# Optimization experiments

Measured on AMD Instinct MI355X. Metric: run time of the kernel, lower is better.

## Reference

```python
import jax, jax.numpy as jnp
import numpy as np

N, E = 10000, 160000          # nodes, edges
MUL = 128                     # channel multiplicity of 0e and 1o blocks
NSP = 10                      # node_attrs (species one-hot) dim
NRAD = 8                      # edge_feats radial basis dim
SILU_C = 1.6790               # e3nn normalize2mom constant for SiLU
AVG_NEIGH = 16.0
SQ3 = np.sqrt(3.0).astype(np.float32)


def setup_inputs() -> dict:
    key = jax.random.key(0)
    ks = jax.random.split(key, 14)
    d = {}
    d["node_feats"] = jax.random.normal(ks[0], (N, 4 * MUL), jnp.float32)   # [N, 128 + 128*3]
    d["node_attrs"] = jax.random.normal(ks[1], (N, NSP), jnp.float32)
    d["edge_feats"] = jax.random.normal(ks[2], (E, NRAD), jnp.float32)
    d["edge_attrs"] = jax.random.normal(ks[3], (E, 4), jnp.float32)          # [0e | 1o]
    d["edge_index"] = jax.random.randint(ks[4], (2, E), 0, N, jnp.int32)
    # e3nn internal weights are standard normal; normalization applied in forward
    d["lin1_ws"] = jax.random.normal(ks[5], (MUL, MUL), jnp.float32)
    d["lin1_wv"] = jax.random.normal(ks[6], (MUL, MUL), jnp.float32)
    d["fc_w0"] = jax.random.normal(ks[7], (NRAD, 64), jnp.float32)
    d["fc_w1"] = jax.random.normal(ks[8], (64, 64), jnp.float32)
    d["fc_w2"] = jax.random.normal(ks[9], (64, 4 * MUL), jnp.float32)        # tp.weight_numel = 512
    d["lin2_ws"] = jax.random.normal(ks[10], (2 * MUL, MUL), jnp.float32)    # 256x0e -> 128x0e
    d["lin2_wv"] = jax.random.normal(ks[11], (2 * MUL, MUL), jnp.float32)    # 256x1o -> 128x1o
    d["sc_ws"] = jax.random.normal(ks[12], (MUL, NSP, MUL), jnp.float32)
    d["sc_wv"] = jax.random.normal(ks[13], (MUL, NSP, MUL), jnp.float32)
    return d


def _fc(ef, w0, w1, w2):
    # e3nn FullyConnectedNet: x @ W / sqrt(fan_in), normalize2mom-scaled SiLU between layers
    h = SILU_C * jax.nn.silu(ef @ w0 / np.float32(np.sqrt(NRAD)))
    h = SILU_C * jax.nn.silu(h @ w1 / np.float32(8.0))
    return h @ w2 / np.float32(8.0)


def reference(node_feats, node_attrs, edge_feats, edge_attrs, edge_index,
              lin1_ws, lin1_wv, fc_w0, fc_w1, fc_w2,
              lin2_ws, lin2_wv, sc_ws, sc_wv):
    x_s = node_feats[:, :MUL]                       # [N, 128] scalar block
    x_v = node_feats[:, MUL:].reshape(N, MUL, 3)    # [N, 128, 3] vector block

    # self-connection: FullyConnectedTensorProduct with 10x0e attrs; path weight 1/sqrt(mul1*mul2)
    sc_norm = np.float32(1.0 / np.sqrt(MUL * NSP))
    sc_s = jnp.einsum('nu,nv,uvw->nw', x_s, node_attrs, sc_ws) * sc_norm
    sc_v = jnp.einsum('nuc,nv,uvw->nwc', x_v, node_attrs, sc_wv) * sc_norm

    # linear_1 (per-irrep channel mixing, fan_in = 128)
    l1 = np.float32(1.0 / np.sqrt(MUL))
    y_s = (x_s @ lin1_ws) * l1
    y_v = jnp.einsum('nuc,uw->nwc', x_v, lin1_wv) * l1

    src = edge_index[1]
    dst = edge_index[0]
    xs_e = y_s[src]                                 # [E, 128]
    xv_e = y_v[src]                                 # [E, 128, 3]
    a_s = edge_attrs[:, :1]                         # [E, 1]
    a_v = edge_attrs[:, 1:]                         # [E, 3]

    w = _fc(edge_feats, fc_w0, fc_w1, fc_w2)        # [E, 512]
    w_ss, w_sv, w_vs, w_vv = jnp.split(w, 4, axis=1)  # instruction order in source

    # 'uvu' weighted tensor product with e3nn component/element normalization:
    # net coefficient per path works out to 1 except 1o x 1o -> 0e which is 1/sqrt(3)
    mid_s0 = w_ss * xs_e * a_s                                          # 0e*0e->0e
    mid_s1 = w_vv * jnp.einsum('euc,ec->eu', xv_e, a_v) / SQ3           # 1o*1o->0e
    mid_v2 = (w_sv * xs_e)[:, :, None] * a_v[:, None, :]                # 0e*1o->1o
    mid_v3 = w_vs[:, :, None] * xv_e * a_s[:, :, None]                  # 1o*0e->1o

    inv = np.float32(1.0 / np.sqrt(AVG_NEIGH))
    s = jax.ops.segment_sum(jnp.concatenate([mid_s0, mid_s1], axis=1), dst, num_segments=N) * inv  # [N, 256]
    v = jax.ops.segment_sum(jnp.concatenate([mid_v2, mid_v3], axis=1), dst, num_segments=N) * inv  # [N, 256, 3]

    # linear_2 (fan_in = 256)
    l2 = np.float32(1.0 / np.sqrt(2 * MUL))
    out_s = (s @ lin2_ws) * l2 + sc_s
    out_v = jnp.einsum('nuc,uw->nwc', v, lin2_wv) * l2 + sc_v

    return jnp.concatenate([out_s, out_v.reshape(N, 3 * MUL)], axis=1)   # [N, 512]
```

## Files before the change

kernel.cpp:

```cpp
#include <hip/hip_runtime.h>
#include <hip/hip_bf16.h>
#include <math.h>

#define N_NODES 10000
#define N_EDGES 160000
#define SO_BLK 157
#define VO_BLK 469

typedef __attribute__((ext_vector_type(8))) short short8x;
typedef __attribute__((ext_vector_type(4))) float floatx4;
typedef __attribute__((ext_vector_type(4))) unsigned int uint4x;
typedef __attribute__((ext_vector_type(2))) unsigned int uint2x;

union S8 { short8x v; unsigned short u[8]; uint4 q; uint4x qx; };
union U2 { uint2x v; unsigned short us[4]; };

__device__ __forceinline__ unsigned short f2bf(float x) {
    unsigned int u = __float_as_uint(x);
    return (unsigned short)((u + 0x7fffu + ((u >> 16) & 1u)) >> 16);
}
__device__ __forceinline__ float bf2f(unsigned short u) {
    return __uint_as_float(((unsigned)u) << 16);
}
__device__ __forceinline__ float silu_c(float x) {
    return 1.679f * x / (1.0f + __expf(-x));
}

__global__ __launch_bounds__(256) void pack_all_kernel(
    const float* __restrict__ sc_ws, const float* __restrict__ lin2_ws,
    const float* __restrict__ sc_wv, const float* __restrict__ lin2_wv,
    const float* __restrict__ fc_w2, const float* __restrict__ fc_w1,
    const float* __restrict__ lin1_ws, const float* __restrict__ lin1_wv,
    unsigned short* __restrict__ b_pre, unsigned short* __restrict__ w2a,
    unsigned short* __restrict__ w1a, unsigned short* __restrict__ b_lin)
{
    const int bid = blockIdx.x;
    const int t = threadIdx.x;
    if (bid < 192) {
        int id = bid * 256 + t;
        int mat = id / 24576;
        int slot = id - mat * 24576;
        int ks = slot >> 9;
        int rr = slot & 511;
        int lane = rr & 63;
        int quad = lane >> 4;
        int n = ((rr >> 6) << 4) + (lane & 15);
        const float* sc  = mat ? sc_wv  : sc_ws;
        const float* lin = mat ? lin2_wv : lin2_ws;
        S8 pk;
        #pragma unroll
        for (int j = 0; j < 8; j++) {
            int k = ks * 32 + quad * 8 + j;
            float w;
            if (k < 1280) {
                int u = k & 127, v = k >> 7;
                w = sc[(u * 10 + v) * 128 + n];
            } else {
                w = lin[(k - 1280) * 128 + n];
            }
            pk.u[j] = f2bf(w);
        }
        *(uint4*)(b_pre + (size_t)id * 8) = pk.q;
    } else if (bid < 208) {
        int id = (bid - 192) * 256 + t;
        int lane = id & 63;
        int mfg = (id >> 6) & 31;
        int ks = id >> 11;
        int col = mfg * 16 + (lane & 15);
        int k0 = ks * 32 + (lane >> 4) * 8;
        S8 pk;
        #pragma unroll
        for (int j = 0; j < 8; j++)
            pk.u[j] = f2bf(fc_w2[(k0 + j) * 512 + col] * 0.125f);
        *(uint4*)(w2a + (size_t)id * 8) = pk.q;
    } else if (bid < 210) {
        int id = (bid - 208) * 256 + t;
        int lane = id & 63;
        int mf = (id >> 6) & 3;
        int ks = id >> 8;
        int m = mf * 16 + (lane & 15);
        int k0 = ks * 32 + (lane >> 4) * 8;
        S8 pk;
        #pragma unroll
        for (int j = 0; j < 8; j++)
            pk.u[j] = f2bf(fc_w1[(k0 + j) * 64 + m] * 0.125f);
        *(uint4*)(w1a + (size_t)id * 8) = pk.q;
    } else {
        int id = (bid - 210) * 256 + t;
        int mat = id >> 11;
        int slot = id & 2047;
        int ks = slot >> 9;
        int rr = slot & 511;
        int nf = rr >> 6;
        int lane = rr & 63;
        int n = nf * 16 + (lane & 15);
        int k0 = ks * 32 + (lane >> 4) * 8;
        const float* w = mat ? lin1_wv : lin1_ws;
        const float l1 = 0.0883883476483f;
        S8 pk;
        #pragma unroll
        for (int j = 0; j < 8; j++)
            pk.u[j] = f2bf(w[(k0 + j) * 128 + n] * l1);
        *(uint4*)(b_lin + (size_t)id * 8) = pk.q;
    }
}

__global__ __launch_bounds__(256) void node_lin1_mfma(
    const float* __restrict__ node_feats,
    const unsigned short* __restrict__ b_lin,
    unsigned short* __restrict__ y_pk,
    unsigned short* __restrict__ xvP16)
{
    __shared__ __align__(16) unsigned char smem[32768];
    short8x* Al = (short8x*)smem;
    unsigned short* Yt = (unsigned short*)smem;

    const int blk = blockIdx.x;
    const int t = threadIdx.x;
    const int base = blk * 32;
    const int lane = t & 63;
    const int wv = t >> 6;
    const int m15 = lane & 15;
    const int k0q = (lane >> 4) * 8;

    #pragma unroll
    for (int it = 0; it < 8; it++) {
        int g = wv * 8 + it;
        int af = g >> 2;
        int ks = g & 3;
        int m = af * 16 + m15;
        int comp = m >> 5;
        int nloc = m & 31;
        int node = base + nloc;
        int valid = (node < N_NODES);
        if (!valid) node = N_NODES - 1;
        int k0 = ks * 32 + k0q;
        const float* row = node_feats + (size_t)node * 512;
        S8 pk;
        if (comp == 0) {
            float4 a = *(const float4*)&row[k0];
            float4 b = *(const float4*)&row[k0 + 4];
            pk.u[0] = f2bf(a.x); pk.u[1] = f2bf(a.y); pk.u[2] = f2bf(a.z); pk.u[3] = f2bf(a.w);
            pk.u[4] = f2bf(b.x); pk.u[5] = f2bf(b.y); pk.u[6] = f2bf(b.z); pk.u[7] = f2bf(b.w);
        } else {
            int c = comp - 1;
            #pragma unroll
            for (int j = 0; j < 8; j++)
                pk.u[j] = f2bf(row[128 + (k0 + j) * 3 + c]);
            if (valid)
                *(uint4*)&xvP16[((size_t)node * 3 + c) * 128 + k0] = pk.q;
        }
        Al[(ks * 8 + af) * 64 + lane] = pk.v;
    }
    __syncthreads();

    floatx4 c[8][2];
    #pragma unroll
    for (int af = 0; af < 8; af++) {
        c[af][0] = (floatx4){0.f, 0.f, 0.f, 0.f};
        c[af][1] = (floatx4){0.f, 0.f, 0.f, 0.f};
    }

    const uint4* bq = (const uint4*)b_lin;
    #pragma unroll
    for (int ks = 0; ks < 4; ks++) {
        S8 bs0, bs1, bv0, bv1;
        bs0.q = bq[       ks*512 + (wv*2+0)*64 + lane];
        bs1.q = bq[       ks*512 + (wv*2+1)*64 + lane];
        bv0.q = bq[2048 + ks*512 + (wv*2+0)*64 + lane];
        bv1.q = bq[2048 + ks*512 + (wv*2+1)*64 + lane];
        #pragma unroll
        for (int af = 0; af < 8; af++) {
            short8x a = Al[(ks*8 + af)*64 + lane];
            if (af < 2) {
                c[af][0] = __builtin_amdgcn_mfma_f32_16x16x32_bf16(a, bs0.v, c[af][0], 0, 0, 0);
                c[af][1] = __builtin_amdgcn_mfma_f32_16x16x32_bf16(a, bs1.v, c[af][1], 0, 0, 0);
            } else {
                c[af][0] = __builtin_amdgcn_mfma_f32_16x16x32_bf16(a, bv0.v, c[af][0], 0, 0, 0);
                c[af][1] = __builtin_amdgcn_mfma_f32_16x16x32_bf16(a, bv1.v, c[af][1], 0, 0, 0);
            }
        }
    }
    __syncthreads();

    {
        const int rq = (lane >> 4) * 4;
        #pragma unroll
        for (int af = 0; af < 8; af++) {
            #pragma unroll
            for (int nf = 0; nf < 2; nf++) {
                int u = wv * 32 + nf * 16 + m15;
                #pragma unroll
                for (int i = 0; i < 4; i++) {
                    int m = af * 16 + rq + i;
                    int comp = m >> 5, nloc = m & 31;
                    Yt[(nloc * 128 + u) * 4 + comp] = f2bf(c[af][nf][i]);
                }
            }
        }
    }
    __syncthreads();
    {
        unsigned short* dst = y_pk + (size_t)base * 512;
        int nrem = N_NODES - base;
        #pragma unroll
        for (int it = 0; it < 8; it++) {
            int idx = it * 256 + t;
            if ((idx >> 6) < nrem)
                *(uint4*)(dst + (size_t)idx * 8) = *(const uint4*)&Yt[idx * 8];
        }
    }
}

__global__ __launch_bounds__(256) void hist_kernel(const int* __restrict__ edge_index,
                                                   int* __restrict__ deg) {
    int e = blockIdx.x * 256 + threadIdx.x;
    if (e < N_EDGES) atomicAdd(&deg[edge_index[e]], 1);
}

__global__ __launch_bounds__(1024) void scan_kernel(const int* __restrict__ deg,
                                                    int* __restrict__ row_start,
                                                    int* __restrict__ cursor) {
    __shared__ int wsum[16];
    __shared__ int carry_s;
    const int t = threadIdx.x;
    const int lane = t & 63, w = t >> 6;
    if (t == 0) carry_s = 0;
    __syncthreads();
    for (int chunk = 0; chunk < 10; chunk++) {
        int idx = chunk * 1024 + t;
        int v = (idx < N_NODES) ? deg[idx] : 0;
        int x = v;
        #pragma unroll
        for (int off = 1; off < 64; off <<= 1) {
            int yv = __shfl_up(x, off, 64);
            if (lane >= off) x += yv;
        }
        if (lane == 63) wsum[w] = x;
        __syncthreads();
        int wpre = 0;
        for (int i = 0; i < w; i++) wpre += wsum[i];
        int incl = x + wpre + carry_s;
        int excl = incl - v;
        if (idx < N_NODES) { row_start[idx] = excl; cursor[idx] = excl; }
        __syncthreads();
        if (t == 1023) carry_s = incl;
        __syncthreads();
    }
    if (t == 0) row_start[N_NODES] = carry_s;
}

__global__ __launch_bounds__(256) void scatter_kernel(const int* __restrict__ edge_index,
                                                      const float* __restrict__ edge_attrs,
                                                      int* __restrict__ cursor,
                                                      int* __restrict__ edge_list,
                                                      int* __restrict__ srcs,
                                                      float* __restrict__ ea_sorted) {
    int e = blockIdx.x * 256 + threadIdx.x;
    if (e < N_EDGES) {
        int pos = atomicAdd(&cursor[edge_index[e]], 1);
        edge_list[pos] = e;
        srcs[pos] = edge_index[N_EDGES + e];
        float4 ea = *(const float4*)(edge_attrs + (size_t)e * 4);
        *(float4*)(ea_sorted + (size_t)pos * 4) = ea;
    }
}

__global__ __launch_bounds__(256) void edge_w_mfma(
    const float* __restrict__ edge_feats,
    const int* __restrict__ edge_list,
    const float* __restrict__ fc_w0,
    const unsigned short* __restrict__ w1a,
    const unsigned short* __restrict__ w2a,
    unsigned short* __restrict__ w_pk)
{
    __shared__ __align__(16) unsigned char smem[26368];
    float* ef = (float*)smem;
    unsigned short* h0b = (unsigned short*)(smem + 2304);
    unsigned short* T   = (unsigned short*)smem;
    unsigned short* h1b = (unsigned short*)(smem + 16896);
    int* eids = (int*)(smem + 26112);

    const int blk = blockIdx.x;
    const int t = threadIdx.x;
    const int eb0 = blk * 64;
    const int lane = t & 63;
    const int wv = t >> 6;
    const int quad = lane >> 4;
    const int m15 = lane & 15;

    if (t < 64) eids[t] = edge_list[eb0 + t];
    __syncthreads();

    #pragma unroll
    for (int r = 0; r < 2; r++) {
        int idx = r * 256 + t;
        int el = idx >> 3;
        int k = idx & 7;
        ef[el * 9 + k] = edge_feats[(size_t)eids[el] * 8 + k];
    }
    __syncthreads();

    {
        const int e_loc = t >> 2;
        const int c0 = (t & 3) * 16;
        float a0[16];
        #pragma unroll
        for (int i = 0; i < 16; i++) a0[i] = 0.f;
        const float* efr = &ef[e_loc * 9];
        #pragma unroll
        for (int k = 0; k < 8; k++) {
            float ek = efr[k];
            float w[16];
            #pragma unroll
            for (int q4 = 0; q4 < 4; q4++)
                *(float4*)&w[q4*4] = *(const float4*)&fc_w0[k*64 + c0 + q4*4];
            #pragma unroll
            for (int i = 0; i < 16; i++) a0[i] += ek * w[i];
        }
        const float is8 = 0.35355339059f;
        S8 p0, p1;
        #pragma unroll
        for (int i = 0; i < 8; i++) {
            p0.u[i] = f2bf(silu_c(a0[i] * is8));
            p1.u[i] = f2bf(silu_c(a0[8 + i] * is8));
        }
        *(uint4*)&h0b[e_loc * 72 + c0]     = p0.q;
        *(uint4*)&h0b[e_loc * 72 + c0 + 8] = p1.q;
    }
    __syncthreads();

    {
        floatx4 c2[4];
        #pragma unroll
        for (int ee = 0; ee < 4; ee++) c2[ee] = (floatx4){0.f, 0.f, 0.f, 0.f};
        const uint4* w1aq = (const uint4*)w1a;
        #pragma unroll
        for (int ks = 0; ks < 2; ks++) {
            S8 afr;
            afr.q = w1aq[(ks*4 + wv)*64 + lane];
            #pragma unroll
            for (int ee = 0; ee < 4; ee++) {
                S8 bfr;
                bfr.q = *(const uint4*)&h0b[(ee*16 + m15) * 72 + ks*32 + quad*8];
                c2[ee] = __builtin_amdgcn_mfma_f32_16x16x32_bf16(afr.v, bfr.v, c2[ee], 0, 0, 0);
            }
        }
        #pragma unroll
        for (int ee = 0; ee < 4; ee++) {
            ushort4 pk = make_ushort4(f2bf(silu_c(c2[ee][0])), f2bf(silu_c(c2[ee][1])),
                                      f2bf(silu_c(c2[ee][2])), f2bf(silu_c(c2[ee][3])));
            *(ushort4*)&h1b[(ee*16 + m15) * 72 + wv*16 + quad*4] = pk;
        }
    }
    __syncthreads();

    const uint4* w2aq = (const uint4*)w2a;
    #pragma unroll 1
    for (int p = 0; p < 4; p++) {
        floatx4 c3[2][4];
        #pragma unroll
        for (int mf = 0; mf < 2; mf++)
            #pragma unroll
            for (int ee = 0; ee < 4; ee++)
                c3[mf][ee] = (floatx4){0.f, 0.f, 0.f, 0.f};

        #pragma unroll
        for (int ks = 0; ks < 2; ks++) {
            S8 bfr[4];
            #pragma unroll
            for (int ee = 0; ee < 4; ee++)
                bfr[ee].q = *(const uint4*)&h1b[(ee*16 + m15) * 72 + ks*32 + quad*8];
            #pragma unroll
            for (int mf = 0; mf < 2; mf++) {
                S8 afr;
                afr.q = w2aq[(size_t)(ks*32 + wv*8 + p*2 + mf) * 64 + lane];
                #pragma unroll
                for (int ee = 0; ee < 4; ee++)
                    c3[mf][ee] = __builtin_amdgcn_mfma_f32_16x16x32_bf16(afr.v, bfr[ee].v, c3[mf][ee], 0, 0, 0);
            }
        }

        __syncthreads();
        #pragma unroll
        for (int mf = 0; mf < 2; mf++) {
            #pragma unroll
            for (int ee = 0; ee < 4; ee++) {
                int e = ee*16 + m15;
                #pragma unroll
                for (int i = 0; i < 4; i++) {
                    int colp = mf*16 + quad*4 + i;
                    T[e*132 + colp*4 + wv] = f2bf(c3[mf][ee][i]);
                }
            }
        }
        __syncthreads();

        #pragma unroll
        for (int it = 0; it < 8; it++) {
            int idx = it * 256 + t;
            int e  = idx >> 5;
            int cu = idx & 31;
            uint2x v = *(const uint2x*)&T[e*132 + cu*4];
            unsigned short* dstp = w_pk + ((size_t)(eb0 + e) * 128 + p*32 + cu) * 4;
            *(uint2x*)dstp = v;
        }
    }
}

__global__ __launch_bounds__(256) void gather_kernel(
    const int* __restrict__ row_start,
    const int* __restrict__ srcs,
    const float* __restrict__ ea_sorted,
    const unsigned short* __restrict__ w_pk,
    const unsigned short* __restrict__ y_pk,
    float* __restrict__ accS,
    float* __restrict__ accV)
{
    const int t = threadIdx.x;
    const int n = blockIdx.x * 4 + (t >> 6);
    const int lane = t & 63;
    const int u0 = lane << 1;

    const int eb = row_start[n];
    const int ee = row_start[n + 1];

    float aS0a=0.f,aS0b=0.f, aS1a=0.f,aS1b=0.f;
    float aV2ax=0.f,aV2ay=0.f,aV2az=0.f, aV2bx=0.f,aV2by=0.f,aV2bz=0.f;
    float aV3ax=0.f,aV3ay=0.f,aV3az=0.f, aV3bx=0.f,aV3by=0.f,aV3bz=0.f;

    auto consume = [&](const S8& w8, const S8& y8, const float4& ea) {
        {
            float wss = bf2f(w8.u[0]), wsv = bf2f(w8.u[1]);
            float wvs = bf2f(w8.u[2]), wvv = bf2f(w8.u[3]);
            float qs = bf2f(y8.u[0]), q0 = bf2f(y8.u[1]), q1 = bf2f(y8.u[2]), q2 = bf2f(y8.u[3]);
            aS0a += wss * qs * ea.x;
            aS1a += wvv * (q0*ea.y + q1*ea.z + q2*ea.w);
            float tsv = wsv * qs;
            aV2ax += tsv * ea.y; aV2ay += tsv * ea.z; aV2az += tsv * ea.w;
            float tvs = wvs * ea.x;
            aV3ax += tvs * q0; aV3ay += tvs * q1; aV3az += tvs * q2;
        }
        {
            float wss = bf2f(w8.u[4]), wsv = bf2f(w8.u[5]);
            float wvs = bf2f(w8.u[6]), wvv = bf2f(w8.u[7]);
            float qs = bf2f(y8.u[4]), q0 = bf2f(y8.u[5]), q1 = bf2f(y8.u[6]), q2 = bf2f(y8.u[7]);
            aS0b += wss * qs * ea.x;
            aS1b += wvv * (q0*ea.y + q1*ea.z + q2*ea.w);
            float tsv = wsv * qs;
            aV2bx += tsv * ea.y; aV2by += tsv * ea.z; aV2bz += tsv * ea.w;
            float tvs = wvs * ea.x;
            aV3bx += tvs * q0; aV3by += tvs * q1; aV3bz += tvs * q2;
        }
    };

    if (eb < ee) {
        const int lastE = ee - 1;
        int j1 = (eb+1 < lastE) ? eb+1 : lastE;
        int sA = srcs[eb];
        int sB = srcs[j1];
        int sP0 = srcs[(eb+2 < lastE) ? eb+2 : lastE];
        int sP1 = srcs[(eb+3 < lastE) ? eb+3 : lastE];

        S8 wA, wB, yA, yB; float4 eaA, eaB;
        wA.qx = __builtin_nontemporal_load((const uint4x*)(w_pk + ((size_t)eb * 128 + u0) * 4));
        eaA   = *(const float4*)(ea_sorted + (size_t)eb * 4);
        yA.q  = *(const uint4*)(y_pk + ((size_t)sA * 128 + u0) * 4);
        wB.qx = __builtin_nontemporal_load((const uint4x*)(w_pk + ((size_t)j1 * 128 + u0) * 4));
        eaB   = *(const float4*)(ea_sorted + (size_t)j1 * 4);
        yB.q  = *(const uint4*)(y_pk + ((size_t)sB * 128 + u0) * 4);

        for (int i = eb; i < ee; i += 2) {
            consume(wA, yA, eaA);
            {
                int jn = (i+2 < lastE) ? i+2 : lastE;
                wA.qx = __builtin_nontemporal_load((const uint4x*)(w_pk + ((size_t)jn * 128 + u0) * 4));
                eaA   = *(const float4*)(ea_sorted + (size_t)jn * 4);
                yA.q  = *(const uint4*)(y_pk + ((size_t)sP0 * 128 + u0) * 4);
                sP0 = srcs[(i+4 < lastE) ? i+4 : lastE];
            }
            if (i + 1 < ee) consume(wB, yB, eaB);
            {
                int jn = (i+3 < lastE) ? i+3 : lastE;
                wB.qx = __builtin_nontemporal_load((const uint4x*)(w_pk + ((size_t)jn * 128 + u0) * 4));
                eaB   = *(const float4*)(ea_sorted + (size_t)jn * 4);
                yB.q  = *(const uint4*)(y_pk + ((size_t)sP1 * 128 + u0) * 4);
                sP1 = srcs[(i+5 < lastE) ? i+5 : lastE];
            }
        }
    }

    const float inv = 0.25f;
    const float s1c = 0.57735026919f * 0.25f;
    *(float2*)(accS + (size_t)n*256 + u0)        = make_float2(aS0a*inv, aS0b*inv);
    *(float2*)(accS + (size_t)n*256 + 128 + u0)  = make_float2(aS1a*s1c, aS1b*s1c);
    *(float2*)(accV + ((size_t)n*3+0)*256 + u0)       = make_float2(aV2ax*inv, aV2bx*inv);
    *(float2*)(accV + ((size_t)n*3+0)*256 + 128 + u0) = make_float2(aV3ax*inv, aV3bx*inv);
    *(float2*)(accV + ((size_t)n*3+1)*256 + u0)       = make_float2(aV2ay*inv, aV2by*inv);
    *(float2*)(accV + ((size_t)n*3+1)*256 + 128 + u0) = make_float2(aV3ay*inv, aV3by*inv);
    *(float2*)(accV + ((size_t)n*3+2)*256 + u0)       = make_float2(aV2az*inv, aV2bz*inv);
    *(float2*)(accV + ((size_t)n*3+2)*256 + 128 + u0) = make_float2(aV3az*inv, aV3bz*inv);
}

__global__ __launch_bounds__(256) void node_out_mfma(
    const float* __restrict__ node_feats,
    const float* __restrict__ node_attrs,
    const unsigned short* __restrict__ xvP16,
    const float* __restrict__ accS,
    const float* __restrict__ accV,
    const unsigned short* __restrict__ b_pre,
    float* __restrict__ out)
{
    __shared__ __align__(16) short8x Abuf[2][256];
    const int bid = blockIdx.x;
    const int t = threadIdx.x;
    const int lane = t & 63;
    const int wv = t >> 6;
    const bool is_s = (bid < SO_BLK);

    const int r    = ((t >> 6) << 4) + (t & 15);
    const int q8   = ((t >> 4) & 3) * 8;

    const float* px = nullptr;
    const unsigned short* pxv = nullptr;
    const float* pa;
    const float* pat;
    if (is_s) {
        int R = bid * 64 + r;
        int node = (R < N_NODES) ? R : 0;
        px  = node_feats + (size_t)node * 512;
        pa  = accS + (size_t)node * 256;
        pat = node_attrs + node * 10;
    } else {
        int Rg = (bid - SO_BLK) * 64 + r;
        if (Rg >= 3 * N_NODES) Rg = 0;
        int node = Rg / 3;
        pxv = xvP16 + (size_t)Rg * 128;
        pa  = accV + (size_t)Rg * 256;
        pat = node_attrs + node * 10;
    }

    const uint4* bb = (const uint4*)(b_pre) + (is_s ? 0 : 24576);
    const float sc_norm = 0.02795084972f;
    const float l2 = 0.0625f;

    float xf[4][8];
    S8    xh[4];
    if (is_s) {
        #pragma unroll
        for (int c = 0; c < 4; c++) {
            floatx4 lo = *(const floatx4*)&px[c*32 + q8];
            floatx4 hi = *(const floatx4*)&px[c*32 + q8 + 4];
            #pragma unroll
            for (int i = 0; i < 4; i++) { xf[c][i] = lo[i]; xf[c][4+i] = hi[i]; }
        }
    } else {
        #pragma unroll
        for (int c = 0; c < 4; c++)
            xh[c].q = *(const uint4*)&pxv[c*32 + q8];
    }
    float attC = pat[0] * sc_norm;

    floatx4 acc[4][2];
    #pragma unroll
    for (int af = 0; af < 4; af++) {
        acc[af][0] = (floatx4){0.f, 0.f, 0.f, 0.f};
        acc[af][1] = (floatx4){0.f, 0.f, 0.f, 0.f};
    }

    const int cof0 = (wv*2+0)*64 + lane;
    const int cof1 = (wv*2+1)*64 + lane;

    auto packx = [&](int c_, float att_) -> short8x {
        S8 pk;
        if (is_s) {
            #pragma unroll
            for (int i = 0; i < 8; i++) pk.u[i] = f2bf(xf[c_][i] * att_);
        } else {
            #pragma unroll
            for (int i = 0; i < 8; i++) pk.u[i] = f2bf(bf2f(xh[c_].u[i]) * att_);
        }
        return pk.v;
    };
    auto mstep = [&](int kb, const S8& b0, const S8& b1) {
        __builtin_amdgcn_s_setprio(1);
        #pragma unroll
        for (int af = 0; af < 4; af++) {
            short8x a = Abuf[kb][af*64 + lane];
            acc[af][0] = __builtin_amdgcn_mfma_f32_16x16x32_bf16(a, b0.v, acc[af][0], 0, 0, 0);
            acc[af][1] = __builtin_amdgcn_mfma_f32_16x16x32_bf16(a, b1.v, acc[af][1], 0, 0, 0);
        }
        __builtin_amdgcn_s_setprio(0);
    };
    auto bload = [&](int k2, S8& b0, S8& b1) {
        b0.q = bb[(size_t)k2*512 + cof0];
        b1.q = bb[(size_t)k2*512 + cof1];
    };
    auto barrier_ = [&]() {
        asm volatile("s_waitcnt lgkmcnt(0)" ::: "memory");
        __builtin_amdgcn_s_barrier();
    };

    S8 bA0, bA1, bB0, bB1;
    bload(0, bA0, bA1);
    bload(1, bB0, bB1);

    Abuf[0][t] = packx(0, attC);
    barrier_();

    #pragma unroll 1
    for (int vb = 0; vb < 9; vb++) {
        float attN = pat[vb + 1] * sc_norm;
        const int ksb = vb * 4;
        Abuf[1][t] = packx(1, attC); mstep(0, bA0, bA1); bload(ksb+2, bA0, bA1); barrier_();
        Abuf[0][t] = packx(2, attC); mstep(1, bB0, bB1); bload(ksb+3, bB0, bB1); barrier_();
        Abuf[1][t] = packx(3, attC); mstep(0, bA0, bA1); bload(ksb+4, bA0, bA1); barrier_();
        Abuf[0][t] = packx(0, attN); mstep(1, bB0, bB1); bload(ksb+5, bB0, bB1); barrier_();
        attC = attN;
    }

    floatx4 aT0[2], aT1[2];
    auto issue0 = [&](int k_) { int j2 = (k_-40)*32 + q8;
        aT0[0] = *(const floatx4*)&pa[j2]; aT0[1] = *(const floatx4*)&pa[j2+4]; };
    auto issue1 = [&](int k_) { int j2 = (k_-40)*32 + q8;
        aT1[0] = *(const floatx4*)&pa[j2]; aT1[1] = *(const floatx4*)&pa[j2+4]; };
    auto packT = [&](const floatx4* a2) -> short8x {
        S8 pk;
        #pragma unroll
        for (int i = 0; i < 4; i++) { pk.u[i] = f2bf(a2[0][i] * l2); pk.u[4+i] = f2bf(a2[1][i] * l2); }
        return pk.v;
    };

    Abuf[1][t] = packx(1, attC); mstep(0, bA0, bA1); bload(38, bA0, bA1); barrier_();
    Abuf[0][t] = packx(2, attC); mstep(1, bB0, bB1); bload(39, bB0, bB1); barrier_();
    issue0(40);
    Abuf[1][t] = packx(3, attC); mstep(0, bA0, bA1); bload(40, bA0, bA1); barrier_();
    issue1(41);
    Abuf[0][t] = packT(aT0); mstep(1, bB0, bB1); bload(41, bB0, bB1); barrier_();
    issue0(42);
    Abuf[1][t] = packT(aT1); mstep(0, bA0, bA1); bload(42, bA0, bA1); barrier_();
    issue1(43);
    Abuf[0][t] = packT(aT0); mstep(1, bB0, bB1); bload(43, bB0, bB1); barrier_();
    issue0(44);
    Abuf[1][t] = packT(aT1); mstep(0, bA0, bA1); bload(44, bA0, bA1); barrier_();
    issue1(45);
    Abuf[0][t] = packT(aT0); mstep(1, bB0, bB1); bload(45, bB0, bB1); barrier_();
    issue0(46);
    Abuf[1][t] = packT(aT1); mstep(0, bA0, bA1); bload(46, bA0, bA1); barrier_();
    issue1(47);
    Abuf[0][t] = packT(aT0); mstep(1, bB0, bB1); bload(47, bB0, bB1); barrier_();
    Abuf[1][t] = packT(aT1); mstep(0, bA0, bA1); barrier_();
    mstep(1, bB0, bB1);

    const int m = lane & 15;
    const int rq = (lane >> 4) * 4;
    if (is_s) {
        const int n0 = bid * 64;
        #pragma unroll
        for (int af = 0; af < 4; af++) {
            #pragma unroll
            for (int i = 0; i < 4; i++) {
                int n = n0 + af*16 + rq + i;
                if (n < N_NODES) {
                    out[(size_t)n*512 + wv*32 + m]      = acc[af][0][i];
                    out[(size_t)n*512 + wv*32 + 16 + m] = acc[af][1][i];
                }
            }
        }
    } else {
        const int r0 = (bid - SO_BLK) * 64;
        #pragma unroll
        for (int af = 0; af < 4; af++) {
            #pragma unroll
            for (int i = 0; i < 4; i++) {
                int Rg = r0 + af*16 + rq + i;
                if (Rg < 3 * N_NODES) {
                    int nn = Rg / 3;
                    int cc = Rg - nn * 3;
                    float* po = out + (size_t)nn*512 + 128 + cc;
                    po[(wv*32 + m)*3]      = acc[af][0][i];
                    po[(wv*32 + 16 + m)*3] = acc[af][1][i];
                }
            }
        }
    }
}

extern "C" void kernel_launch(void* const* d_in, const int* in_sizes, int n_in,
                              void* d_out, int out_size, void* d_ws, size_t ws_size,
                              hipStream_t stream) {
    const float* node_feats = (const float*)d_in[0];
    const float* node_attrs = (const float*)d_in[1];
    const float* edge_feats = (const float*)d_in[2];
    const float* edge_attrs = (const float*)d_in[3];
    const int*   edge_index = (const int*)  d_in[4];
    const float* lin1_ws    = (const float*)d_in[5];
    const float* lin1_wv    = (const float*)d_in[6];
    const float* fc_w0      = (const float*)d_in[7];
    const float* fc_w1      = (const float*)d_in[8];
    const float* fc_w2      = (const float*)d_in[9];
    const float* lin2_ws    = (const float*)d_in[10];
    const float* lin2_wv    = (const float*)d_in[11];
    const float* sc_ws      = (const float*)d_in[12];
    const float* sc_wv      = (const float*)d_in[13];
    float* out = (float*)d_out;

    unsigned short* y_pk  = (unsigned short*)d_ws;
    float* accS = (float*)(y_pk + (size_t)5120000);
    float* accV = accS + (size_t)2560000;
    unsigned short* xvP16 = (unsigned short*)(accV + (size_t)7680000);
    unsigned short* w_pk  = xvP16 + (size_t)3840000;
    int* deg       = (int*)(w_pk + (size_t)81920000);
    int* row_start = deg + 10016;
    int* cursor    = row_start + 10016;
    int* edge_list = cursor + 10016;
    int* srcs      = edge_list + N_EDGES;
    float* ea_sorted = (float*)(srcs + N_EDGES);
    unsigned short* b_pre = (unsigned short*)(ea_sorted + (size_t)N_EDGES * 4);
    unsigned short* w2a   = b_pre + (size_t)2 * 24576 * 8;
    unsigned short* w1a   = w2a + (size_t)4096 * 8;
    unsigned short* b_lin = w1a + (size_t)512 * 8;
    const size_t need = (size_t)5120000 * 2 + (size_t)(2560000 + 7680000) * 4
                      + (size_t)3840000 * 2 + (size_t)81920000 * 2
                      + (size_t)(10016 * 3 + N_EDGES * 2) * 4
                      + (size_t)N_EDGES * 4 * 4
                      + ((size_t)2 * 24576 * 8 + (size_t)4096 * 8 + (size_t)512 * 8
                         + (size_t)4096 * 8) * 2;
    if (ws_size < need) return;

    hipLaunchKernelGGL(pack_all_kernel, dim3(226), dim3(256), 0, stream,
                       sc_ws, lin2_ws, sc_wv, lin2_wv, fc_w2, fc_w1, lin1_ws, lin1_wv,
                       b_pre, w2a, w1a, b_lin);
    hipLaunchKernelGGL(node_lin1_mfma, dim3(313), dim3(256), 0, stream,
                       node_feats, b_lin, y_pk, xvP16);

    hipMemsetAsync(deg, 0, (size_t)N_NODES * sizeof(int), stream);
    hipLaunchKernelGGL(hist_kernel, dim3(625), dim3(256), 0, stream, edge_index, deg);
    hipLaunchKernelGGL(scan_kernel, dim3(1), dim3(1024), 0, stream, deg, row_start, cursor);
    hipLaunchKernelGGL(scatter_kernel, dim3(625), dim3(256), 0, stream,
                       edge_index, edge_attrs, cursor, edge_list, srcs, ea_sorted);
    hipLaunchKernelGGL(edge_w_mfma, dim3(2500), dim3(256), 0, stream,
                       edge_feats, edge_list, fc_w0, w1a, w2a, w_pk);
    hipLaunchKernelGGL(gather_kernel, dim3(2500), dim3(256), 0, stream,
                       row_start, srcs, ea_sorted, w_pk, y_pk, accS, accV);

    hipLaunchKernelGGL(node_out_mfma, dim3(SO_BLK + VO_BLK), dim3(256), 0, stream,
                       node_feats, node_attrs, xvP16, accS, accV, b_pre, out);
}
```

Measured before the change: 282.9 us.

## Fuse edge radial MLP with message aggregation via segmented atomics, dropping w_pk buffer

The per-edge tensor-product weights are no longer written to a large bf16 global buffer and re-read by a separate gather kernel. The edge MLP kernel now computes the messages straight from its shared-memory weight tile and accumulates them per destination node in registers, runs of equal destination are flushed with float atomics into zeroed accumulators, and the 1/sqrt(avg_neigh) and 1/sqrt(3) scaling moves into the output linear's pack step. This removes a write and read of roughly 160 MB of intermediate data, at the cost of many global atomics, a memset of the accumulators, and summation order that varies from run to run.

```diff
diff --git a/kernel.cpp b/kernel.cpp
--- a/kernel.cpp
+++ b/kernel.cpp
@@ -13,7 +13,6 @@
 typedef __attribute__((ext_vector_type(2))) unsigned int uint2x;
 
 union S8 { short8x v; unsigned short u[8]; uint4 q; uint4x qx; };
-union U2 { uint2x v; unsigned short us[4]; };
 
 __device__ __forceinline__ unsigned short f2bf(float x) {
     unsigned int u = __float_as_uint(x);
@@ -255,12 +254,15 @@
                                                       int* __restrict__ cursor,
                                                       int* __restrict__ edge_list,
                                                       int* __restrict__ srcs,
+                                                      int* __restrict__ dsts,
                                                       float* __restrict__ ea_sorted) {
     int e = blockIdx.x * 256 + threadIdx.x;
     if (e < N_EDGES) {
-        int pos = atomicAdd(&cursor[edge_index[e]], 1);
+        int dd = edge_index[e];
+        int pos = atomicAdd(&cursor[dd], 1);
         edge_list[pos] = e;
         srcs[pos] = edge_index[N_EDGES + e];
+        dsts[pos] = dd;
         float4 ea = *(const float4*)(edge_attrs + (size_t)e * 4);
         *(float4*)(ea_sorted + (size_t)pos * 4) = ea;
     }
@@ -269,17 +271,25 @@
 __global__ __launch_bounds__(256) void edge_w_mfma(
     const float* __restrict__ edge_feats,
     const int* __restrict__ edge_list,
+    const int* __restrict__ srcs,
+    const int* __restrict__ dsts,
+    const float* __restrict__ ea_sorted,
     const float* __restrict__ fc_w0,
     const unsigned short* __restrict__ w1a,
     const unsigned short* __restrict__ w2a,
-    unsigned short* __restrict__ w_pk)
+    const unsigned short* __restrict__ y_pk,
+    float* __restrict__ accS,
+    float* __restrict__ accV)
 {
-    __shared__ __align__(16) unsigned char smem[26368];
+    __shared__ __align__(16) unsigned char smem[27904];
     float* ef = (float*)smem;
     unsigned short* h0b = (unsigned short*)(smem + 2304);
     unsigned short* T   = (unsigned short*)smem;
     unsigned short* h1b = (unsigned short*)(smem + 16896);
-    int* eids = (int*)(smem + 26112);
+    int* eids   = (int*)(smem + 26112);
+    int* srcs_l = (int*)(smem + 26368);
+    int* dsts_l = (int*)(smem + 26624);
+    float* ea_l = (float*)(smem + 26880);
 
     const int blk = blockIdx.x;
     const int t = threadIdx.x;
@@ -289,7 +299,12 @@
     const int quad = lane >> 4;
     const int m15 = lane & 15;
 
-    if (t < 64) eids[t] = edge_list[eb0 + t];
+    if (t < 64) {
+        eids[t]   = edge_list[eb0 + t];
+        srcs_l[t] = srcs[eb0 + t];
+        dsts_l[t] = dsts[eb0 + t];
+    }
+    ea_l[t] = ea_sorted[(size_t)eb0 * 4 + t];
     __syncthreads();
 
     #pragma unroll
@@ -396,110 +411,57 @@
         }
         __syncthreads();
 
-        #pragma unroll
-        for (int it = 0; it < 8; it++) {
-            int idx = it * 256 + t;
-            int e  = idx >> 5;
-            int cu = idx & 31;
-            uint2x v = *(const uint2x*)&T[e*132 + cu*4];
-            unsigned short* dstp = w_pk + ((size_t)(eb0 + e) * 128 + p*32 + cu) * 4;
-            *(uint2x*)dstp = v;
-        }
-    }
-}
-
-__global__ __launch_bounds__(256) void gather_kernel(
-    const int* __restrict__ row_start,
-    const int* __restrict__ srcs,
-    const float* __restrict__ ea_sorted,
-    const unsigned short* __restrict__ w_pk,
-    const unsigned short* __restrict__ y_pk,
-    float* __restrict__ accS,
-    float* __restrict__ accV)
-{
-    const int t = threadIdx.x;
-    const int n = blockIdx.x * 4 + (t >> 6);
-    const int lane = t & 63;
-    const int u0 = lane << 1;
-
-    const int eb = row_start[n];
-    const int ee = row_start[n + 1];
-
-    float aS0a=0.f,aS0b=0.f, aS1a=0.f,aS1b=0.f;
-    float aV2ax=0.f,aV2ay=0.f,aV2az=0.f, aV2bx=0.f,aV2by=0.f,aV2bz=0.f;
-    float aV3ax=0.f,aV3ay=0.f,aV3az=0.f, aV3bx=0.f,aV3by=0.f,aV3bz=0.f;
-
-    auto consume = [&](const S8& w8, const S8& y8, const float4& ea) {
         {
-            float wss = bf2f(w8.u[0]), wsv = bf2f(w8.u[1]);
-            float wvs = bf2f(w8.u[2]), wvv = bf2f(w8.u[3]);
-            float qs = bf2f(y8.u[0]), q0 = bf2f(y8.u[1]), q1 = bf2f(y8.u[2]), q2 = bf2f(y8.u[3]);
-            aS0a += wss * qs * ea.x;
-            aS1a += wvv * (q0*ea.y + q1*ea.z + q2*ea.w);
-            float tsv = wsv * qs;
-            aV2ax += tsv * ea.y; aV2ay += tsv * ea.z; aV2az += tsv * ea.w;
-            float tvs = wvs * ea.x;
-            aV3ax += tvs * q0; aV3ay += tvs * q1; aV3az += tvs * q2;
-        }
-        {
-            float wss = bf2f(w8.u[4]), wsv = bf2f(w8.u[5]);
-            float wvs = bf2f(w8.u[6]), wvv = bf2f(w8.u[7]);
-            float qs = bf2f(y8.u[4]), q0 = bf2f(y8.u[5]), q1 = bf2f(y8.u[6]), q2 = bf2f(y8.u[7]);
-            aS0b += wss * qs * ea.x;
-            aS1b += wvv * (q0*ea.y + q1*ea.z + q2*ea.w);
-            float tsv = wsv * qs;
-            aV2bx += tsv * ea.y; aV2by += tsv * ea.z; aV2bz += tsv * ea.w;
-            float tvs = wvs * ea.x;
-            aV3bx += tvs * q0; aV3by += tvs * q1; aV3bz += tvs * q2;
-        }
-    };
-
-    if (eb < ee) {
-        const int lastE = ee - 1;
-        int j1 = (eb+1 < lastE) ? eb+1 : lastE;
-        int sA = srcs[eb];
-        int sB = srcs[j1];
-        int sP0 = srcs[(eb+2 < lastE) ? eb+2 : lastE];
-        int sP1 = srcs[(eb+3 < lastE) ? eb+3 : lastE];
-
-        S8 wA, wB, yA, yB; float4 eaA, eaB;
-        wA.qx = __builtin_nontemporal_load((const uint4x*)(w_pk + ((size_t)eb * 128 + u0) * 4));
-        eaA   = *(const float4*)(ea_sorted + (size_t)eb * 4);
-        yA.q  = *(const uint4*)(y_pk + ((size_t)sA * 128 + u0) * 4);
-        wB.qx = __builtin_nontemporal_load((const uint4x*)(w_pk + ((size_t)j1 * 128 + u0) * 4));
-        eaB   = *(const float4*)(ea_sorted + (size_t)j1 * 4);
-        yB.q  = *(const uint4*)(y_pk + ((size_t)sB * 128 + u0) * 4);
-
-        for (int i = eb; i < ee; i += 2) {
-            consume(wA, yA, eaA);
-            {
-                int jn = (i+2 < lastE) ? i+2 : lastE;
-                wA.qx = __builtin_nontemporal_load((const uint4x*)(w_pk + ((size_t)jn * 128 + u0) * 4));
-                eaA   = *(const float4*)(ea_sorted + (size_t)jn * 4);
-                yA.q  = *(const uint4*)(y_pk + ((size_t)sP0 * 128 + u0) * 4);
-                sP0 = srcs[(i+4 < lastE) ? i+4 : lastE];
-            }
-            if (i + 1 < ee) consume(wB, yB, eaB);
-            {
-                int jn = (i+3 < lastE) ? i+3 : lastE;
-                wB.qx = __builtin_nontemporal_load((const uint4x*)(w_pk + ((size_t)jn * 128 + u0) * 4));
-                eaB   = *(const float4*)(ea_sorted + (size_t)jn * 4);
-                yB.q  = *(const uint4*)(y_pk + ((size_t)sP1 * 128 + u0) * 4);
-                sP1 = srcs[(i+5 < lastE) ? i+5 : lastE];
-            }
-        }
-    }
-
-    const float inv = 0.25f;
-    const float s1c = 0.57735026919f * 0.25f;
-    *(float2*)(accS + (size_t)n*256 + u0)        = make_float2(aS0a*inv, aS0b*inv);
-    *(float2*)(accS + (size_t)n*256 + 128 + u0)  = make_float2(aS1a*s1c, aS1b*s1c);
-    *(float2*)(accV + ((size_t)n*3+0)*256 + u0)       = make_float2(aV2ax*inv, aV2bx*inv);
-    *(float2*)(accV + ((size_t)n*3+0)*256 + 128 + u0) = make_float2(aV3ax*inv, aV3bx*inv);
-    *(float2*)(accV + ((size_t)n*3+1)*256 + u0)       = make_float2(aV2ay*inv, aV2by*inv);
-    *(float2*)(accV + ((size_t)n*3+1)*256 + 128 + u0) = make_float2(aV3ay*inv, aV3by*inv);
-    *(float2*)(accV + ((size_t)n*3+2)*256 + u0)       = make_float2(aV2az*inv, aV2bz*inv);
-    *(float2*)(accV + ((size_t)n*3+2)*256 + 128 + u0) = make_float2(aV3az*inv, aV3bz*inv);
+            const int u_loc = t & 31;
+            const int g8 = (t >> 5) * 8;
+            const int u = p * 32 + u_loc;
+
+            float aS0=0.f, aS1=0.f;
+            float aV2x=0.f, aV2y=0.f, aV2z=0.f;
+            float aV3x=0.f, aV3y=0.f, aV3z=0.f;
+
+            auto flushn = [&](int nd) {
+                atomicAdd(&accS[(size_t)nd*256 + u], aS0);
+                atomicAdd(&accS[(size_t)nd*256 + 128 + u], aS1);
+                atomicAdd(&accV[((size_t)nd*3+0)*256 + u], aV2x);
+                atomicAdd(&accV[((size_t)nd*3+0)*256 + 128 + u], aV3x);
+                atomicAdd(&accV[((size_t)nd*3+1)*256 + u], aV2y);
+                atomicAdd(&accV[((size_t)nd*3+1)*256 + 128 + u], aV3y);
+                atomicAdd(&accV[((size_t)nd*3+2)*256 + u], aV2z);
+                atomicAdd(&accV[((size_t)nd*3+2)*256 + 128 + u], aV3z);
+                aS0=aS1=0.f; aV2x=aV2y=aV2z=0.f; aV3x=aV3y=aV3z=0.f;
+            };
+
+            int curd = dsts_l[g8];
+            ushort4 w4 = *(const ushort4*)&T[g8*132 + u_loc*4];
+            ushort4 y4 = *(const ushort4*)(y_pk + ((size_t)srcs_l[g8]*128 + u)*4);
+
+            #pragma unroll
+            for (int j = 0; j < 8; j++) {
+                int jn = (j < 7) ? (g8 + j + 1) : (g8 + 7);
+                ushort4 w4n = *(const ushort4*)&T[jn*132 + u_loc*4];
+                ushort4 y4n = *(const ushort4*)(y_pk + ((size_t)srcs_l[jn]*128 + u)*4);
+
+                int d = dsts_l[g8 + j];
+                if (d != curd) { flushn(curd); curd = d; }
+
+                float ex = ea_l[(g8+j)*4+0], ey = ea_l[(g8+j)*4+1];
+                float ez = ea_l[(g8+j)*4+2], ew = ea_l[(g8+j)*4+3];
+                float wss = bf2f(w4.x), wsv = bf2f(w4.y);
+                float wvs = bf2f(w4.z), wvv = bf2f(w4.w);
+                float qs = bf2f(y4.x), q0 = bf2f(y4.y), q1 = bf2f(y4.z), q2 = bf2f(y4.w);
+                aS0 += wss * qs * ex;
+                aS1 += wvv * (q0*ey + q1*ez + q2*ew);
+                float tsv = wsv * qs;
+                aV2x += tsv * ey; aV2y += tsv * ez; aV2z += tsv * ew;
+                float tvs = wvs * ex;
+                aV3x += tvs * q0; aV3y += tvs * q1; aV3z += tvs * q2;
+
+                w4 = w4n; y4 = y4n;
+            }
+            flushn(curd);
+        }
+    }
 }
 
 __global__ __launch_bounds__(256) void node_out_mfma(
@@ -542,7 +504,8 @@
 
     const uint4* bb = (const uint4*)(b_pre) + (is_s ? 0 : 24576);
     const float sc_norm = 0.02795084972f;
-    const float l2 = 0.0625f;
+    const float scLo = 0.015625f;
+    const float scHi = is_s ? 0.00902110898f : 0.015625f;
 
     float xf[4][8];
     S8    xh[4];
@@ -624,10 +587,10 @@
         aT0[0] = *(const floatx4*)&pa[j2]; aT0[1] = *(const floatx4*)&pa[j2+4]; };
     auto issue1 = [&](int k_) { int j2 = (k_-40)*32 + q8;
         aT1[0] = *(const floatx4*)&pa[j2]; aT1[1] = *(const floatx4*)&pa[j2+4]; };
-    auto packT = [&](const floatx4* a2) -> short8x {
+    auto packT = [&](const floatx4* a2, float sc) -> short8x {
         S8 pk;
         #pragma unroll
-        for (int i = 0; i < 4; i++) { pk.u[i] = f2bf(a2[0][i] * l2); pk.u[4+i] = f2bf(a2[1][i] * l2); }
+        for (int i = 0; i < 4; i++) { pk.u[i] = f2bf(a2[0][i] * sc); pk.u[4+i] = f2bf(a2[1][i] * sc); }
         return pk.v;
     };
 
@@ -636,20 +599,20 @@
     issue0(40);
     Abuf[1][t] = packx(3, attC); mstep(0, bA0, bA1); bload(40, bA0, bA1); barrier_();
     issue1(41);
-    Abuf[0][t] = packT(aT0); mstep(1, bB0, bB1); bload(41, bB0, bB1); barrier_();
+    Abuf[0][t] = packT(aT0, scLo); mstep(1, bB0, bB1); bload(41, bB0, bB1); barrier_();
     issue0(42);
-    Abuf[1][t] = packT(aT1); mstep(0, bA0, bA1); bload(42, bA0, bA1); barrier_();
+    Abuf[1][t] = packT(aT1, scLo); mstep(0, bA0, bA1); bload(42, bA0, bA1); barrier_();
     issue1(43);
-    Abuf[0][t] = packT(aT0); mstep(1, bB0, bB1); bload(43, bB0, bB1); barrier_();
+    Abuf[0][t] = packT(aT0, scLo); mstep(1, bB0, bB1); bload(43, bB0, bB1); barrier_();
     issue0(44);
-    Abuf[1][t] = packT(aT1); mstep(0, bA0, bA1); bload(44, bA0, bA1); barrier_();
+    Abuf[1][t] = packT(aT1, scLo); mstep(0, bA0, bA1); bload(44, bA0, bA1); barrier_();
     issue1(45);
-    Abuf[0][t] = packT(aT0); mstep(1, bB0, bB1); bload(45, bB0, bB1); barrier_();
+    Abuf[0][t] = packT(aT0, scHi); mstep(1, bB0, bB1); bload(45, bB0, bB1); barrier_();
     issue0(46);
-    Abuf[1][t] = packT(aT1); mstep(0, bA0, bA1); bload(46, bA0, bA1); barrier_();
+    Abuf[1][t] = packT(aT1, scHi); mstep(0, bA0, bA1); bload(46, bA0, bA1); barrier_();
     issue1(47);
-    Abuf[0][t] = packT(aT0); mstep(1, bB0, bB1); bload(47, bB0, bB1); barrier_();
-    Abuf[1][t] = packT(aT1); mstep(0, bA0, bA1); barrier_();
+    Abuf[0][t] = packT(aT0, scHi); mstep(1, bB0, bB1); bload(47, bB0, bB1); barrier_();
+    Abuf[1][t] = packT(aT1, scHi); mstep(0, bA0, bA1); barrier_();
     mstep(1, bB0, bB1);
 
     const int m = lane & 15;
@@ -709,24 +672,27 @@
     float* accS = (float*)(y_pk + (size_t)5120000);
     float* accV = accS + (size_t)2560000;
     unsigned short* xvP16 = (unsigned short*)(accV + (size_t)7680000);
-    unsigned short* w_pk  = xvP16 + (size_t)3840000;
-    int* deg       = (int*)(w_pk + (size_t)81920000);
+    int* deg       = (int*)(xvP16 + (size_t)3840000);
     int* row_start = deg + 10016;
     int* cursor    = row_start + 10016;
     int* edge_list = cursor + 10016;
     int* srcs      = edge_list + N_EDGES;
-    float* ea_sorted = (float*)(srcs + N_EDGES);
+    int* dsts      = srcs + N_EDGES;
+    float* ea_sorted = (float*)(dsts + N_EDGES);
     unsigned short* b_pre = (unsigned short*)(ea_sorted + (size_t)N_EDGES * 4);
     unsigned short* w2a   = b_pre + (size_t)2 * 24576 * 8;
     unsigned short* w1a   = w2a + (size_t)4096 * 8;
     unsigned short* b_lin = w1a + (size_t)512 * 8;
     const size_t need = (size_t)5120000 * 2 + (size_t)(2560000 + 7680000) * 4
-                      + (size_t)3840000 * 2 + (size_t)81920000 * 2
-                      + (size_t)(10016 * 3 + N_EDGES * 2) * 4
+                      + (size_t)3840000 * 2
+                      + (size_t)(10016 * 3 + N_EDGES * 3) * 4
                       + (size_t)N_EDGES * 4 * 4
                       + ((size_t)2 * 24576 * 8 + (size_t)4096 * 8 + (size_t)512 * 8
                          + (size_t)4096 * 8) * 2;
     if (ws_size < need) return;
+
+    hipMemsetAsync(accS, 0, (size_t)(2560000 + 7680000) * sizeof(float), stream);
+    hipMemsetAsync(deg, 0, (size_t)N_NODES * sizeof(int), stream);
 
     hipLaunchKernelGGL(pack_all_kernel, dim3(226), dim3(256), 0, stream,
                        sc_ws, lin2_ws, sc_wv, lin2_wv, fc_w2, fc_w1, lin1_ws, lin1_wv,
@@ -734,15 +700,13 @@
     hipLaunchKernelGGL(node_lin1_mfma, dim3(313), dim3(256), 0, stream,
                        node_feats, b_lin, y_pk, xvP16);
 
-    hipMemsetAsync(deg, 0, (size_t)N_NODES * sizeof(int), stream);
     hipLaunchKernelGGL(hist_kernel, dim3(625), dim3(256), 0, stream, edge_index, deg);
     hipLaunchKernelGGL(scan_kernel, dim3(1), dim3(1024), 0, stream, deg, row_start, cursor);
     hipLaunchKernelGGL(scatter_kernel, dim3(625), dim3(256), 0, stream,
-                       edge_index, edge_attrs, cursor, edge_list, srcs, ea_sorted);
+                       edge_index, edge_attrs, cursor, edge_list, srcs, dsts, ea_sorted);
     hipLaunchKernelGGL(edge_w_mfma, dim3(2500), dim3(256), 0, stream,
-                       edge_feats, edge_list, fc_w0, w1a, w2a, w_pk);
-    hipLaunchKernelGGL(gather_kernel, dim3(2500), dim3(256), 0, stream,
-                       row_start, srcs, ea_sorted, w_pk, y_pk, accS, accV);
+                       edge_feats, edge_list, srcs, dsts, ea_sorted,
+                       fc_w0, w1a, w2a, y_pk, accS, accV);
 
     hipLaunchKernelGGL(node_out_mfma, dim3(SO_BLK + VO_BLK), dim3(256), 0, stream,
                        node_feats, node_attrs, xvP16, accS, accV, b_pre, out);
```

After: 348.8 us. +23.3%, slower.
